# Kernel tuning notes

Measured on AMD Instinct MI355X. Metric: run time of the kernel, lower is better.

The kernel has to match this reference:

```python
import jax, jax.numpy as jnp
import numpy as np
import math

IN_C, N_EMBD, HEADS = 256, 512, 8

def setup_inputs() -> dict:
    key = jax.random.key(0)
    ks = jax.random.split(key, 5)
    B, T = 64, 500
    x = jax.random.normal(ks[0], (B, T, IN_C), dtype=jnp.float32)
    # torch Linear: y = x @ W.T + b; store W as [out, in]
    w_attn = jax.random.normal(ks[1], (3 * N_EMBD, IN_C), dtype=jnp.float32) * (1.0 / math.sqrt(IN_C))
    b_attn = jax.random.normal(ks[2], (3 * N_EMBD,), dtype=jnp.float32) * 0.02
    w_proj = jax.random.normal(ks[3], (N_EMBD, N_EMBD), dtype=jnp.float32) * (1.0 / math.sqrt(N_EMBD))
    b_proj = jax.random.normal(ks[4], (N_EMBD,), dtype=jnp.float32) * 0.02
    return {"x": x, "w_attn": w_attn, "b_attn": b_attn, "w_proj": w_proj, "b_proj": b_proj}

def reference(x, w_attn, b_attn, w_proj, b_proj):
    B, T, C = x.shape
    H, D = HEADS, N_EMBD // HEADS
    qkv = jnp.einsum('btc,ec->bte', x, w_attn) + b_attn  # [B,T,3*n_embd]
    q, k, v = jnp.split(qkv, 3, axis=-1)
    # [B,T,n_embd] -> [B,H,T,D]
    q = q.reshape(B, T, H, D).transpose(0, 2, 1, 3)
    k = k.reshape(B, T, H, D).transpose(0, 2, 1, 3)
    v = v.reshape(B, T, H, D).transpose(0, 2, 1, 3)
    att = jnp.einsum('bhtd,bhsd->bhts', q, k) * (1.0 / math.sqrt(D))
    # bias buffer is all-ones: masked_fill(bias==0, -inf) is a no-op
    att = jax.nn.softmax(att, axis=-1)
    y = jnp.einsum('bhts,bhsd->bhtd', att, v)  # [B,H,T,D]
    y = y.transpose(0, 2, 1, 3).reshape(B, T, N_EMBD)
    return jnp.einsum('bte,fe->btf', y, w_proj) + b_proj
```

## Files before the change

kernel.cpp:

```cpp
#include <hip/hip_runtime.h>

typedef _Float16 f16;
typedef _Float16 f16x8 __attribute__((ext_vector_type(8)));
typedef _Float16 f16x4 __attribute__((ext_vector_type(4)));
typedef _Float16 f16x2 __attribute__((ext_vector_type(2)));
typedef float    f32x4 __attribute__((ext_vector_type(4)));
typedef float    f32x16 __attribute__((ext_vector_type(16)));
typedef unsigned int u32;

typedef const __attribute__((address_space(1))) void GVOID;
typedef __attribute__((address_space(3))) void LVOID;

static __device__ __forceinline__ f32x16 mfma32(f16x8 a, f16x8 b, f32x16 c) {
  return __builtin_amdgcn_mfma_f32_32x32x16_f16(a, b, c, 0, 0, 0);
}
static __device__ __forceinline__ void gl_lds16(const f16* g, f16* l) {
  __builtin_amdgcn_global_load_lds((GVOID*)g, (LVOID*)l, 16, 0, 0);
}
static __device__ __forceinline__ u32 pk(float a, float b) {
  union { f16x2 h; u32 w; } u;
  u.h[0] = (f16)a; u.h[1] = (f16)b;
  return u.w;
}
static __device__ __forceinline__ u32 pkh(f16 a, f16 b) {
  union { f16x2 h; u32 w; } u;
  u.h[0] = a; u.h[1] = b;
  return u.w;
}
static __device__ __forceinline__ f16x8 mkfrag(float a0, float a1, float a2, float a3,
                                               float a4, float a5, float a6, float a7) {
  u32 c01 = pk(a0, a1), c23 = pk(a2, a3), c45 = pk(a4, a5), c67 = pk(a6, a7);
  asm("v_permlane32_swap_b32 %0, %1" : "+v"(c01), "+v"(c45));
  asm("v_permlane32_swap_b32 %0, %1" : "+v"(c23), "+v"(c67));
  union { f16x8 h; u32 w[4]; } u;
  u.w[0] = c01; u.w[1] = c23; u.w[2] = c45; u.w[3] = c67;
  return u.h;
}

__global__ __launch_bounds__(256)
void cvt_all(const float* __restrict__ x,  f16* __restrict__ xh,
             const float* __restrict__ wa, f16* __restrict__ wah,
             const float* __restrict__ wp, f16* __restrict__ wph) {
  int i = (blockIdx.x * 256 + threadIdx.x) * 8;
  const float* s; f16* d;
  if (i < 8192000)            { s = x + i;                 d = xh + i; }
  else if (i < 8192000+393216){ int j = i - 8192000;       s = wa + j; d = wah + j; }
  else                        { int j = i - 8585216;       s = wp + j; d = wph + j; }
  float4 v0 = *(const float4*)(s);
  float4 v1 = *(const float4*)(s + 4);
  f16x8 h;
  h[0] = (f16)v0.x; h[1] = (f16)v0.y; h[2] = (f16)v0.z; h[3] = (f16)v0.w;
  h[4] = (f16)v1.x; h[5] = (f16)v1.y; h[6] = (f16)v1.z; h[7] = (f16)v1.w;
  *(f16x8*)d = h;
}

template<int EPI, int KD, int NDIM>
__global__ __launch_bounds__(512)
void gemm256(const f16* __restrict__ A, const f16* __restrict__ B,
             const float* __restrict__ bias, f16* __restrict__ outH,
             float* __restrict__ outF) {
  constexpr int NB = NDIM / 128;
  const int nwg = gridDim.x;
  const int orig = blockIdx.x;
  const int xcd = orig & 7, loc = orig >> 3;
  const int qq = nwg >> 3, rr8 = nwg & 7;
  const int g = (xcd < rr8 ? xcd * (qq + 1) : rr8 * (qq + 1) + (xcd - rr8) * qq) + loc;
  const int mb = g / NB, nb = g - mb * NB;
  const int m0 = mb * 256, n0 = nb * 128;

  __shared__ __align__(16) f16 As[256 * 64];
  __shared__ __align__(16) f16 Bs[128 * 64];
  const int tid = threadIdx.x, wid = tid >> 6;
  const int l31 = tid & 31, hi = (tid >> 5) & 1;
  const int wm = (wid >> 1) * 64, wn = (wid & 1) * 64;

  f32x16 acc[2][2] = {};

  for (int k0 = 0; k0 < KD; k0 += 64) {
    __syncthreads();
#pragma unroll
    for (int i = 0; i < 4; ++i) {
      int c = i * 512 + tid, row = c >> 3;
      int col = 8 * ((c & 7) ^ (row & 7));
      gl_lds16(A + (size_t)(m0 + row) * KD + k0 + col, &As[c * 8]);
    }
#pragma unroll
    for (int i = 0; i < 2; ++i) {
      int c = i * 512 + tid, row = c >> 3;
      int col = 8 * ((c & 7) ^ (row & 7));
      gl_lds16(B + (size_t)(n0 + row) * KD + k0 + col, &Bs[c * 8]);
    }
    __syncthreads();
#pragma unroll
    for (int kk = 0; kk < 4; ++kk) {
      f16x8 af[2], bf[2];
#pragma unroll
      for (int t = 0; t < 2; ++t) {
        int ra = wm + t * 32 + l31;
        af[t] = *(const f16x8*)&As[ra * 64 + 8 * ((2 * kk + hi) ^ (ra & 7))];
        int rb = wn + t * 32 + l31;
        bf[t] = *(const f16x8*)&Bs[rb * 64 + 8 * ((2 * kk + hi) ^ (rb & 7))];
      }
#pragma unroll
      for (int ms = 0; ms < 2; ++ms)
#pragma unroll
        for (int ns = 0; ns < 2; ++ns)
          acc[ms][ns] = mfma32(af[ms], bf[ns], acc[ms][ns]);
    }
  }

  float bv[2];
  bv[0] = bias[n0 + wn + l31];
  bv[1] = bias[n0 + wn + 32 + l31];
#pragma unroll
  for (int ms = 0; ms < 2; ++ms)
#pragma unroll
    for (int ns = 0; ns < 2; ++ns)
#pragma unroll
      for (int r = 0; r < 16; ++r) {
        int mrow = (r & 3) + 8 * (r >> 2) + 4 * hi;
        int m_g = m0 + wm + ms * 32 + mrow;
        int n_g = n0 + wn + ns * 32 + l31;
        float v = acc[ms][ns][r] + bv[ns];
        if (EPI == 0) outH[(size_t)m_g * NDIM + n_g] = (f16)v;
        else          outF[(size_t)m_g * NDIM + n_g] = v;
      }
}

__global__ __launch_bounds__(512, 4)
void attn_kern(const f16* __restrict__ qkv, f16* __restrict__ Yg) {
  __shared__ __align__(16) f16 Kl[2][64 * 64];
  __shared__ __align__(16) f16 VT[2][64 * 64];
  const int id = blockIdx.x;
  const int g = (id & 7) * 128 + (id >> 3);
  const int bh = g >> 1, qt = g & 1;
  const int b = bh >> 3, h = bh & 7;
  const int tid = threadIdx.x, w = tid >> 6;
  const int l31 = tid & 31, hi = (tid & 63) >> 5, e7 = l31 & 7;

  const f16* base  = qkv + (size_t)b * 500 * 1536 + h * 64;
  const f16* Kbase = base + 512;
  const f16* Vbase = base + 1024;

  const int q = qt * 256 + w * 32 + l31;
  const int qc = q < 500 ? q : 499;
  f16x8 qf[4];
  const f16* qp = base + (size_t)qc * 1536 + hi * 8;
#pragma unroll
  for (int ds = 0; ds < 4; ++ds) qf[ds] = *(const f16x8*)(qp + 16 * ds);
  const f16 qs = (f16)(0.125f * 1.44269504f);
#pragma unroll
  for (int ds = 0; ds < 4; ++ds)
#pragma unroll
    for (int j = 0; j < 8; ++j) qf[ds][j] *= qs;

  f32x16 O0 = {}, O1 = {};
  float l = 0.f;

  const int krow = tid >> 3, kcol = 8 * ((tid & 7) ^ (krow & 7));
  const int kvp = (tid & 31) * 2, d4 = (tid >> 5) * 4;
  f16x4 va, vb;
  const f16x4 VZ4 = {};

  {
    gl_lds16(Kbase + (size_t)krow * 1536 + kcol, &Kl[0][tid * 8]);
    const f16* vp0 = Vbase + (size_t)kvp * 1536 + d4;
    va = *(const f16x4*)vp0; vb = *(const f16x4*)(vp0 + 1536);
#pragma unroll
    for (int dd = 0; dd < 4; ++dd) {
      int d = d4 + dd;
      *(u32*)&VT[0][d * 64 + (kvp ^ ((d & 7) << 3))] = pkh(va[dd], vb[dd]);
    }
    __syncthreads();
  }

#pragma unroll 2
  for (int kt = 0; kt < 8; ++kt) {
    const int cur = kt & 1, nxt = cur ^ 1;
    if (kt < 7) {
      const int kvn = (kt + 1) * 64;
      int kr = kvn + krow; kr = kr < 500 ? kr : 499;
      gl_lds16(Kbase + (size_t)kr * 1536 + kcol, &Kl[nxt][tid * 8]);
      int kv = kvn + kvp;
      int kc0 = kv < 500 ? kv : 499, kc1 = kv + 1 < 500 ? kv + 1 : 499;
      va = *(const f16x4*)(Vbase + (size_t)kc0 * 1536 + d4);
      vb = *(const f16x4*)(Vbase + (size_t)kc1 * 1536 + d4);
      if (kv >= 500) va = VZ4;
      if (kv + 1 >= 500) vb = VZ4;
    }

    f32x16 s0 = {}, s1 = {};
    __builtin_amdgcn_s_setprio(1);
#pragma unroll
    for (int ds = 0; ds < 4; ++ds) {
      f16x8 k0 = *(const f16x8*)&Kl[cur][l31 * 64 + 8 * ((hi + 2 * ds) ^ e7)];
      f16x8 k1 = *(const f16x8*)&Kl[cur][(32 + l31) * 64 + 8 * ((hi + 2 * ds) ^ e7)];
      s0 = mfma32(k0, qf[ds], s0);
      s1 = mfma32(k1, qf[ds], s1);
    }
    __builtin_amdgcn_s_setprio(0);

    if (kt == 7) {
#pragma unroll
      for (int r = 0; r < 16; ++r) {
        int kvL = (r & 3) + 8 * (r >> 2) + 4 * hi;
        if (480 + kvL >= 500) s1[r] = -1e30f;
      }
    }

    float ps = 0.f;
#pragma unroll
    for (int r = 0; r < 16; ++r) {
      float t = __builtin_amdgcn_exp2f(s0[r]);
      s0[r] = t; ps += t;
    }
#pragma unroll
    for (int r = 0; r < 16; ++r) {
      float t = __builtin_amdgcn_exp2f(s1[r]);
      s1[r] = t; ps += t;
    }
    ps += __shfl_xor(ps, 32);
    l += ps;

    f16x8 pf0 = mkfrag(s0[0], s0[1], s0[2], s0[3], s0[4], s0[5], s0[6], s0[7]);
    f16x8 pf1 = mkfrag(s0[8], s0[9], s0[10], s0[11], s0[12], s0[13], s0[14], s0[15]);
    f16x8 pf2 = mkfrag(s1[0], s1[1], s1[2], s1[3], s1[4], s1[5], s1[6], s1[7]);
    f16x8 pf3 = mkfrag(s1[8], s1[9], s1[10], s1[11], s1[12], s1[13], s1[14], s1[15]);

    __builtin_amdgcn_s_setprio(1);
#pragma unroll
    for (int ks = 0; ks < 4; ++ks) {
      f16x8 pf = ks == 0 ? pf0 : ks == 1 ? pf1 : ks == 2 ? pf2 : pf3;
      int sw = (16 * ks + 8 * hi) ^ (e7 << 3);
      f16x8 v0 = *(const f16x8*)&VT[cur][l31 * 64 + sw];
      f16x8 v1 = *(const f16x8*)&VT[cur][(32 + l31) * 64 + sw];
      O0 = mfma32(pf, v0, O0);
      O1 = mfma32(pf, v1, O1);
    }
    __builtin_amdgcn_s_setprio(0);

    if (kt < 7) {
#pragma unroll
      for (int dd = 0; dd < 4; ++dd) {
        int d = d4 + dd;
        *(u32*)&VT[nxt][d * 64 + (kvp ^ ((d & 7) << 3))] = pkh(va[dd], vb[dd]);
      }
    }
    __syncthreads();
  }

  float linv = __builtin_amdgcn_rcpf(l);
#pragma unroll
  for (int r = 0; r < 16; ++r) {
    int rowv = (r & 3) + 8 * (r >> 2) + 4 * hi;
    float li = __shfl(linv, rowv);
    int t = qt * 256 + w * 32 + rowv;
    if (t < 500) {
      size_t rowb = (size_t)(b * 500 + t) * 512 + h * 64;
      Yg[rowb + l31]      = (f16)(O0[r] * li);
      Yg[rowb + 32 + l31] = (f16)(O1[r] * li);
    }
  }
}

extern "C" void kernel_launch(void* const* d_in, const int* in_sizes, int n_in,
                              void* d_out, int out_size, void* d_ws, size_t ws_size,
                              hipStream_t stream) {
  const float* x      = (const float*)d_in[0];
  const float* w_attn = (const float*)d_in[1];
  const float* b_attn = (const float*)d_in[2];
  const float* w_proj = (const float*)d_in[3];
  const float* b_proj = (const float*)d_in[4];
  float* out = (float*)d_out;

  char* wsp = (char*)d_ws;
  f16* Yg   = (f16*)wsp;
  f16* x_h  = (f16*)wsp;
  f16* qkv  = (f16*)(wsp + 32768000);
  f16* wa_h = (f16*)(wsp + 32768000 + 98304000);
  f16* wp_h = (f16*)(wsp + 32768000 + 98304000 + 786432);
  if (ws_size < 132382720) return;

  cvt_all<<<4320, dim3(256), 0, stream>>>(x, x_h, w_attn, wa_h, w_proj, wp_h);

  gemm256<0, 256, 1536><<<1500, dim3(512), 0, stream>>>(x_h, wa_h, b_attn, qkv, nullptr);
  attn_kern<<<1024, dim3(512), 0, stream>>>(qkv, Yg);
  gemm256<1, 512, 512><<<500, dim3(512), 0, stream>>>(Yg, wp_h, b_proj, nullptr, out);
}
```

Before: 136.3 us.

## Triple-buffer GEMM K-tiles with explicit vmcnt waits and ping-pong barriers

Rewrites both linear-layer GEMM kernels to prefetch two K-tiles ahead into a three-slot LDS ring, using explicit s_waitcnt vmcnt counts in place of the two __syncthreads per iteration. The warp tiling changes from 64x64 per wave to 128x32, so each wave issues four MFMAs per k-step sharing a single B fragment. Extra s_barrier calls and s_setprio around the MFMA groups try to keep the waves in lockstep. The cost is triple the LDS footprint (about 144KB), which limits occupancy, plus many more barriers per iteration.

```diff
diff --git a/kernel.cpp b/kernel.cpp
--- a/kernel.cpp
+++ b/kernel.cpp
@@ -4,7 +4,6 @@
 typedef _Float16 f16x8 __attribute__((ext_vector_type(8)));
 typedef _Float16 f16x4 __attribute__((ext_vector_type(4)));
 typedef _Float16 f16x2 __attribute__((ext_vector_type(2)));
-typedef float    f32x4 __attribute__((ext_vector_type(4)));
 typedef float    f32x16 __attribute__((ext_vector_type(16)));
 typedef unsigned int u32;
 
@@ -56,75 +55,98 @@
 
 template<int EPI, int KD, int NDIM>
 __global__ __launch_bounds__(512)
-void gemm256(const f16* __restrict__ A, const f16* __restrict__ B,
-             const float* __restrict__ bias, f16* __restrict__ outH,
-             float* __restrict__ outF) {
-  constexpr int NB = NDIM / 128;
-  const int nwg = gridDim.x;
-  const int orig = blockIdx.x;
+void gemm8p(const f16* __restrict__ A, const f16* __restrict__ B,
+            const float* __restrict__ bias, f16* __restrict__ outH,
+            float* __restrict__ outF) {
+  constexpr int KT = KD / 64;
+  constexpr int ABUF = 256 * 64, BBUF = 128 * 64, BUFSZ = ABUF + BBUF;
+  __shared__ __align__(16) f16 lds[3 * BUFSZ];
+
+  const int nwg = gridDim.x, orig = blockIdx.x;
   const int xcd = orig & 7, loc = orig >> 3;
   const int qq = nwg >> 3, rr8 = nwg & 7;
-  const int g = (xcd < rr8 ? xcd * (qq + 1) : rr8 * (qq + 1) + (xcd - rr8) * qq) + loc;
-  const int mb = g / NB, nb = g - mb * NB;
+  const int gb = (xcd < rr8 ? xcd * (qq + 1) : rr8 * (qq + 1) + (xcd - rr8) * qq) + loc;
+  constexpr int NB = NDIM / 128;
+  const int mb = gb / NB, nb = gb - mb * NB;
   const int m0 = mb * 256, n0 = nb * 128;
 
-  __shared__ __align__(16) f16 As[256 * 64];
-  __shared__ __align__(16) f16 Bs[128 * 64];
   const int tid = threadIdx.x, wid = tid >> 6;
   const int l31 = tid & 31, hi = (tid >> 5) & 1;
-  const int wm = (wid >> 1) * 64, wn = (wid & 1) * 64;
-
-  f32x16 acc[2][2] = {};
-
-  for (int k0 = 0; k0 < KD; k0 += 64) {
-    __syncthreads();
+  const int wm = (wid >> 2) * 128, wn = (wid & 3) * 32;
+
+  f32x16 acc[4] = {};
+
+  auto STAGE = [&](int t) {
+    const int k0 = t * 64;
+    f16* Ab = &lds[(t % 3) * BUFSZ];
+    f16* Bb = Ab + ABUF;
 #pragma unroll
     for (int i = 0; i < 4; ++i) {
       int c = i * 512 + tid, row = c >> 3;
       int col = 8 * ((c & 7) ^ (row & 7));
-      gl_lds16(A + (size_t)(m0 + row) * KD + k0 + col, &As[c * 8]);
+      gl_lds16(A + (size_t)(m0 + row) * KD + k0 + col, &Ab[c * 8]);
     }
 #pragma unroll
     for (int i = 0; i < 2; ++i) {
       int c = i * 512 + tid, row = c >> 3;
       int col = 8 * ((c & 7) ^ (row & 7));
-      gl_lds16(B + (size_t)(n0 + row) * KD + k0 + col, &Bs[c * 8]);
-    }
-    __syncthreads();
+      gl_lds16(B + (size_t)(n0 + row) * KD + k0 + col, &Bb[c * 8]);
+    }
+  };
+
+  STAGE(0);
+  STAGE(1);
+
+#pragma unroll
+  for (int t = 0; t < KT; ++t) {
+    if (t + 2 < KT) STAGE(t + 2);
+    if (t < KT - 2)       asm volatile("s_waitcnt vmcnt(12)" ::: "memory");
+    else if (t == KT - 2) asm volatile("s_waitcnt vmcnt(6)"  ::: "memory");
+    else                  asm volatile("s_waitcnt vmcnt(0)"  ::: "memory");
+    __builtin_amdgcn_sched_barrier(0);
+    __builtin_amdgcn_s_barrier();
+    __builtin_amdgcn_sched_barrier(0);
+
+    const f16* Ab = &lds[(t % 3) * BUFSZ];
+    const f16* Bb = Ab + ABUF;
 #pragma unroll
     for (int kk = 0; kk < 4; ++kk) {
-      f16x8 af[2], bf[2];
-#pragma unroll
-      for (int t = 0; t < 2; ++t) {
-        int ra = wm + t * 32 + l31;
-        af[t] = *(const f16x8*)&As[ra * 64 + 8 * ((2 * kk + hi) ^ (ra & 7))];
-        int rb = wn + t * 32 + l31;
-        bf[t] = *(const f16x8*)&Bs[rb * 64 + 8 * ((2 * kk + hi) ^ (rb & 7))];
+      f16x8 af[4], bf;
+      {
+        int rb = wn + l31;
+        bf = *(const f16x8*)&Bb[rb * 64 + 8 * ((2 * kk + hi) ^ (rb & 7))];
       }
 #pragma unroll
-      for (int ms = 0; ms < 2; ++ms)
-#pragma unroll
-        for (int ns = 0; ns < 2; ++ns)
-          acc[ms][ns] = mfma32(af[ms], bf[ns], acc[ms][ns]);
+      for (int ms = 0; ms < 4; ++ms) {
+        int ra = wm + ms * 32 + l31;
+        af[ms] = *(const f16x8*)&Ab[ra * 64 + 8 * ((2 * kk + hi) ^ (ra & 7))];
+      }
+      __builtin_amdgcn_sched_barrier(0);
+      __builtin_amdgcn_s_barrier();
+      __builtin_amdgcn_sched_barrier(0);
+      __builtin_amdgcn_s_setprio(1);
+#pragma unroll
+      for (int ms = 0; ms < 4; ++ms)
+        acc[ms] = mfma32(af[ms], bf, acc[ms]);
+      __builtin_amdgcn_s_setprio(0);
+      __builtin_amdgcn_sched_barrier(0);
+      __builtin_amdgcn_s_barrier();
+      __builtin_amdgcn_sched_barrier(0);
     }
   }
 
-  float bv[2];
-  bv[0] = bias[n0 + wn + l31];
-  bv[1] = bias[n0 + wn + 32 + l31];
-#pragma unroll
-  for (int ms = 0; ms < 2; ++ms)
-#pragma unroll
-    for (int ns = 0; ns < 2; ++ns)
-#pragma unroll
-      for (int r = 0; r < 16; ++r) {
-        int mrow = (r & 3) + 8 * (r >> 2) + 4 * hi;
-        int m_g = m0 + wm + ms * 32 + mrow;
-        int n_g = n0 + wn + ns * 32 + l31;
-        float v = acc[ms][ns][r] + bv[ns];
-        if (EPI == 0) outH[(size_t)m_g * NDIM + n_g] = (f16)v;
-        else          outF[(size_t)m_g * NDIM + n_g] = v;
-      }
+  float bv = bias[n0 + wn + l31];
+#pragma unroll
+  for (int ms = 0; ms < 4; ++ms)
+#pragma unroll
+    for (int r = 0; r < 16; ++r) {
+      int mrow = (r & 3) + 8 * (r >> 2) + 4 * hi;
+      int m_g = m0 + wm + ms * 32 + mrow;
+      int n_g = n0 + wn + l31;
+      float v = acc[ms][r] + bv;
+      if (EPI == 0) outH[(size_t)m_g * NDIM + n_g] = (f16)v;
+      else          outF[(size_t)m_g * NDIM + n_g] = v;
+    }
 }
 
 __global__ __launch_bounds__(512, 4)
@@ -283,7 +305,7 @@
 
   cvt_all<<<4320, dim3(256), 0, stream>>>(x, x_h, w_attn, wa_h, w_proj, wp_h);
 
-  gemm256<0, 256, 1536><<<1500, dim3(512), 0, stream>>>(x_h, wa_h, b_attn, qkv, nullptr);
+  gemm8p<0, 256, 1536><<<1500, dim3(512), 0, stream>>>(x_h, wa_h, b_attn, qkv, nullptr);
   attn_kern<<<1024, dim3(512), 0, stream>>>(qkv, Yg);
-  gemm256<1, 512, 512><<<500, dim3(512), 0, stream>>>(Yg, wp_h, b_proj, nullptr, out);
-}
+  gemm8p<1, 512, 512><<<500, dim3(512), 0, stream>>>(Yg, wp_h, b_proj, nullptr, out);
+}
```

Result: slower. 142.6 us (+4.6%).
